# Optimization experiments

Hardware: AMD Instinct MI355X
Metric: run time of the kernel (lower is better)

The kernel has to match this reference:

```python
import jax, jax.numpy as jnp
import numpy as np

B, H, Q, K = 2, 12, 2048, 2048
D, NPOS = 128, 512


def setup_inputs() -> dict:
    key = jax.random.key(0)
    k1, k2, k3 = jax.random.split(key, 3)
    return {
        "query": jax.random.normal(k1, (B, H, Q, D), dtype=jnp.float32),
        "attn_logits": jax.random.normal(k2, (B, H, Q, K), dtype=jnp.float32),
        "pos_emb": jax.random.normal(k3, (1, D, NPOS), dtype=jnp.float32),
        "npos_max": NPOS,
    }


def reference(query, attn_logits, pos_emb, npos_max):
    # CoPE, 1D (H=None) branch.
    gates = jax.nn.sigmoid(attn_logits)                       # [b,h,q,k]
    # reversed cumsum along keys: position of each key counted from the right
    pos = jnp.flip(jnp.cumsum(jnp.flip(gates, axis=-1), axis=-1), axis=-1)
    pos = jnp.minimum(pos, jnp.float32(npos_max - 1))
    pos_ceil = jnp.ceil(pos).astype(jnp.int32)                # [b,h,q,k]
    pos_floor = jnp.floor(pos).astype(jnp.int32)
    # query @ pos_emb -> interpolation table over integer positions
    logits_int = jnp.einsum("bhqd,dn->bhqn", query, pos_emb[0])  # [b,h,q,npos]
    logits_ceil = jnp.take_along_axis(logits_int, pos_ceil, axis=-1)
    logits_floor = jnp.take_along_axis(logits_int, pos_floor, axis=-1)
    w = pos - pos_floor.astype(pos.dtype)
    return logits_ceil * w + logits_floor * (1.0 - w)
```

## Files before the change

kernel.cpp:

```cpp
#include <hip/hip_runtime.h>
#include <math.h>

#define DD    128
#define NPOS  512
#define KK    2048
#define RPB   16
#define BLK   1024

typedef __attribute__((ext_vector_type(8))) short short8_t;
typedef __attribute__((ext_vector_type(4))) float f32x4;

union BfPack {
    unsigned u[4];
    short8_t v;
};

__device__ __forceinline__ float sigmoidf_fast(float x) {
    return __builtin_amdgcn_rcpf(1.0f + __expf(-x));
}

__device__ __forceinline__ unsigned pack_bf16(float lo, float hi) {
    return (__float_as_uint(hi) & 0xffff0000u) | (__float_as_uint(lo) >> 16);
}

__global__ __launch_bounds__(BLK, 8)
void cope_kernel(const float* __restrict__ query,
                 const float* __restrict__ attn,
                 const float* __restrict__ pos_emb,
                 const int*   __restrict__ npos_max_p,
                 float* __restrict__ out)
{
    const int t    = threadIdx.x;
    const int wv   = t >> 6;
    const int lane = t & 63;

    __shared__ float s_tab[RPB][NPOS + 1];

    const size_t row_base = (size_t)blockIdx.x * RPB;

    {
        const int m  = lane & 15;
        const int g  = lane >> 4;
        const int n0 = wv * 32 + m;

        f32x4 acc0 = {0.f, 0.f, 0.f, 0.f};
        f32x4 acc1 = {0.f, 0.f, 0.f, 0.f};

        #pragma unroll
        for (int kk = 0; kk < 4; ++kk) {
            const int k0 = kk * 32 + g * 8;

            const float* qp = query + (row_base + m) * DD + k0;
            f32x4 a0 = *reinterpret_cast<const f32x4*>(qp);
            f32x4 a1 = *reinterpret_cast<const f32x4*>(qp + 4);
            BfPack af;
            af.u[0] = pack_bf16(a0.x, a0.y);
            af.u[1] = pack_bf16(a0.z, a0.w);
            af.u[2] = pack_bf16(a1.x, a1.y);
            af.u[3] = pack_bf16(a1.z, a1.w);

            const float* bp = pos_emb + (size_t)k0 * NPOS + n0;
            float b0[8], b1[8];
            #pragma unroll
            for (int j = 0; j < 8; ++j) {
                b0[j] = bp[(size_t)j * NPOS];
                b1[j] = bp[(size_t)j * NPOS + 16];
            }
            BfPack bf0, bf1;
            #pragma unroll
            for (int j = 0; j < 4; ++j) {
                bf0.u[j] = pack_bf16(b0[2 * j], b0[2 * j + 1]);
                bf1.u[j] = pack_bf16(b1[2 * j], b1[2 * j + 1]);
            }

            acc0 = __builtin_amdgcn_mfma_f32_16x16x32_bf16(af.v, bf0.v, acc0, 0, 0, 0);
            acc1 = __builtin_amdgcn_mfma_f32_16x16x32_bf16(af.v, bf1.v, acc1, 0, 0, 0);
        }

        #pragma unroll
        for (int r = 0; r < 4; ++r) {
            s_tab[g * 4 + r][n0]      = acc0[r];
            s_tab[g * 4 + r][n0 + 16] = acc1[r];
        }
        if (t < RPB) s_tab[t][NPOS] = 0.0f;
    }
    __syncthreads();

    {
        float lo[8], hi[8];
        #pragma unroll
        for (int j = 0; j < 8; ++j) {
            const int e = lane + j * 64;
            lo[j] = s_tab[wv][e];
            hi[j] = s_tab[wv][e + 1];
        }
        __syncthreads();
        unsigned* urow = reinterpret_cast<unsigned*>(s_tab[wv]);
        #pragma unroll
        for (int j = 0; j < 8; ++j)
            urow[lane + j * 64] = pack_bf16(lo[j], hi[j]);
    }
    __syncthreads();

    const size_t row = row_base + wv;
    const float* arow = attn + row * (size_t)KK;
    float*       orow = out  + row * (size_t)KK;
    const unsigned* utab = reinterpret_cast<const unsigned*>(s_tab[wv]);

    const float clampv = (float)(*npos_max_p - 1);

    float suff[8][4];
    float lct[8];
    float incl[8];

    #pragma unroll
    for (int c = 0; c < 8; ++c) {
        f32x4 gv = *reinterpret_cast<const f32x4*>(arow + c * 256 + lane * 4);
        float s0 = sigmoidf_fast(gv.x);
        float s1 = sigmoidf_fast(gv.y);
        float s2 = sigmoidf_fast(gv.z);
        float s3 = sigmoidf_fast(gv.w);
        suff[c][3] = s3;
        suff[c][2] = s2 + suff[c][3];
        suff[c][1] = s1 + suff[c][2];
        suff[c][0] = s0 + suff[c][1];
        lct[c] = suff[c][0];

        float v = lct[c];
        #pragma unroll
        for (int off = 1; off < 64; off <<= 1) {
            float u = __shfl_down(v, off);
            if (lane + off < 64) v += u;
        }
        incl[c] = v;
    }

    float Tc[8];
    #pragma unroll
    for (int c = 0; c < 8; ++c) Tc[c] = __shfl(incl[c], 0);
    float offc[8];
    offc[7] = 0.0f;
    #pragma unroll
    for (int c = 6; c >= 0; --c) offc[c] = offc[c + 1] + Tc[c + 1];

    #pragma unroll
    for (int c = 0; c < 8; ++c) {
        float base = offc[c] + (incl[c] - lct[c]);
        f32x4 res;
        #pragma unroll
        for (int j = 0; j < 4; ++j) {
            float pos = fminf(suff[c][j] + base, clampv);
            int   ifl = (int)pos;
            float wgt = pos - (float)ifl;
            unsigned u = utab[ifl];
            float lf = __uint_as_float(u << 16);
            float lc = __uint_as_float(u & 0xffff0000u);
            res[j] = fmaf(wgt, lc - lf, lf);
        }
        __builtin_nontemporal_store(res, reinterpret_cast<f32x4*>(orow + c * 256 + lane * 4));
    }
}

extern "C" void kernel_launch(void* const* d_in, const int* in_sizes, int n_in,
                              void* d_out, int out_size, void* d_ws, size_t ws_size,
                              hipStream_t stream) {
    const float* query   = (const float*)d_in[0];
    const float* attn    = (const float*)d_in[1];
    const float* pos_emb = (const float*)d_in[2];
    const int*   nposp   = (const int*)d_in[3];
    float*       outp    = (float*)d_out;

    const int rows   = in_sizes[1] / KK;
    const int blocks = rows / RPB;

    cope_kernel<<<blocks, BLK, 0, stream>>>(query, attn, pos_emb, nposp, outp);
}
```

Measured before the change: 169.0 us.

## Process six row groups per block with double-buffered GEMM table pipelining

Each block now handles six groups of 16 rows instead of one. The query×pos_emb MFMA for the next group is computed while the current group runs its scan and gather, using double-buffered LDS tables. This cuts block launch count and overlaps GEMM work with memory-bound output. The in-place bf16 pack now happens with no barrier between its reads and writes, and only one __syncthreads runs per iteration. This may race across waves, since each wave reads e+1 from its own row only, so it is probably fine. The grid shrinks to 49152/96 = 512 blocks, which lowers parallelism on a 256-CU device.

```diff
diff --git a/kernel.cpp b/kernel.cpp
--- a/kernel.cpp
+++ b/kernel.cpp
@@ -6,6 +6,8 @@
 #define KK    2048
 #define RPB   16
 #define BLK   1024
+#define GPB   6
+#define LROW  (NPOS + 1)
 
 typedef __attribute__((ext_vector_type(8))) short short8_t;
 typedef __attribute__((ext_vector_type(4))) float f32x4;
@@ -34,21 +36,25 @@
     const int wv   = t >> 6;
     const int lane = t & 63;
 
-    __shared__ float s_tab[RPB][NPOS + 1];
+    __shared__ float s_tab[2][RPB][LROW];
 
-    const size_t row_base = (size_t)blockIdx.x * RPB;
+    const size_t blk_row0 = (size_t)blockIdx.x * (RPB * GPB);
 
-    {
-        const int m  = lane & 15;
-        const int g  = lane >> 4;
-        const int n0 = wv * 32 + m;
+    const int m   = lane & 15;
+    const int g16 = lane >> 4;
+    const int n0  = wv * 32 + m;
 
-        f32x4 acc0 = {0.f, 0.f, 0.f, 0.f};
-        f32x4 acc1 = {0.f, 0.f, 0.f, 0.f};
+    const float clampv = (float)(*npos_max_p - 1);
 
+    f32x4 acc0, acc1;
+
+    auto gemm_compute = [&](int grp) {
+        const size_t row_base = blk_row0 + (size_t)grp * RPB;
+        acc0 = (f32x4){0.f, 0.f, 0.f, 0.f};
+        acc1 = (f32x4){0.f, 0.f, 0.f, 0.f};
         #pragma unroll
         for (int kk = 0; kk < 4; ++kk) {
-            const int k0 = kk * 32 + g * 8;
+            const int k0 = kk * 32 + g16 * 8;
 
             const float* qp = query + (row_base + m) * DD + k0;
             f32x4 a0 = *reinterpret_cast<const f32x4*>(qp);
@@ -76,88 +82,101 @@
             acc0 = __builtin_amdgcn_mfma_f32_16x16x32_bf16(af.v, bf0.v, acc0, 0, 0, 0);
             acc1 = __builtin_amdgcn_mfma_f32_16x16x32_bf16(af.v, bf1.v, acc1, 0, 0, 0);
         }
+    };
+
+    auto gemm_store = [&](int buf) {
+        #pragma unroll
+        for (int r = 0; r < 4; ++r) {
+            s_tab[buf][g16 * 4 + r][n0]      = acc0[r];
+            s_tab[buf][g16 * 4 + r][n0 + 16] = acc1[r];
+        }
+        if (t < RPB) s_tab[buf][t][NPOS] = 0.0f;
+    };
+
+    gemm_compute(0);
+    gemm_store(0);
+
+    #pragma unroll 1
+    for (int g = 0; g < GPB; ++g) {
+        const int cur = g & 1;
+
+        if (g + 1 < GPB) gemm_compute(g + 1);
+
+        __syncthreads();
+
+        if (g + 1 < GPB) gemm_store(cur ^ 1);
+
+        float* tabf = s_tab[cur][wv];
+        {
+            float lo[8], hi[8];
+            #pragma unroll
+            for (int j = 0; j < 8; ++j) {
+                const int e = lane + j * 64;
+                lo[j] = tabf[e];
+                hi[j] = tabf[e + 1];
+            }
+            unsigned* urow = reinterpret_cast<unsigned*>(tabf);
+            #pragma unroll
+            for (int j = 0; j < 8; ++j)
+                urow[lane + j * 64] = pack_bf16(lo[j], hi[j]);
+        }
+
+        const size_t row  = blk_row0 + (size_t)g * RPB + wv;
+        const float* arow = attn + row * (size_t)KK;
+        float*       orow = out  + row * (size_t)KK;
+        const unsigned* utab = reinterpret_cast<const unsigned*>(tabf);
+
+        float suff[8][4];
+        float lct[8];
+        float incl[8];
 
         #pragma unroll
-        for (int r = 0; r < 4; ++r) {
-            s_tab[g * 4 + r][n0]      = acc0[r];
-            s_tab[g * 4 + r][n0 + 16] = acc1[r];
+        for (int c = 0; c < 8; ++c) {
+            f32x4 gv = *reinterpret_cast<const f32x4*>(arow + c * 256 + lane * 4);
+            float s0 = sigmoidf_fast(gv.x);
+            float s1 = sigmoidf_fast(gv.y);
+            float s2 = sigmoidf_fast(gv.z);
+            float s3 = sigmoidf_fast(gv.w);
+            suff[c][3] = s3;
+            suff[c][2] = s2 + suff[c][3];
+            suff[c][1] = s1 + suff[c][2];
+            suff[c][0] = s0 + suff[c][1];
+            lct[c] = suff[c][0];
+
+            float v = lct[c];
+            #pragma unroll
+            for (int off = 1; off < 64; off <<= 1) {
+                float u = __shfl_down(v, off);
+                if (lane + off < 64) v += u;
+            }
+            incl[c] = v;
         }
-        if (t < RPB) s_tab[t][NPOS] = 0.0f;
-    }
-    __syncthreads();
 
-    {
-        float lo[8], hi[8];
+        float Tc[8];
         #pragma unroll
-        for (int j = 0; j < 8; ++j) {
-            const int e = lane + j * 64;
-            lo[j] = s_tab[wv][e];
-            hi[j] = s_tab[wv][e + 1];
+        for (int c = 0; c < 8; ++c) Tc[c] = __shfl(incl[c], 0);
+        float offc[8];
+        offc[7] = 0.0f;
+        #pragma unroll
+        for (int c = 6; c >= 0; --c) offc[c] = offc[c + 1] + Tc[c + 1];
+
+        #pragma unroll
+        for (int c = 0; c < 8; ++c) {
+            float base = offc[c] + (incl[c] - lct[c]);
+            f32x4 res;
+            #pragma unroll
+            for (int j = 0; j < 4; ++j) {
+                float pos = fminf(suff[c][j] + base, clampv);
+                int   ifl = (int)pos;
+                float wgt = pos - (float)ifl;
+                unsigned u = utab[ifl];
+                float lf = __uint_as_float(u << 16);
+                float lc = __uint_as_float(u & 0xffff0000u);
+                res[j] = fmaf(wgt, lc - lf, lf);
+            }
+            __builtin_nontemporal_store(res,
+                reinterpret_cast<f32x4*>(orow + c * 256 + lane * 4));
         }
-        __syncthreads();
-        unsigned* urow = reinterpret_cast<unsigned*>(s_tab[wv]);
-        #pragma unroll
-        for (int j = 0; j < 8; ++j)
-            urow[lane + j * 64] = pack_bf16(lo[j], hi[j]);
-    }
-    __syncthreads();
-
-    const size_t row = row_base + wv;
-    const float* arow = attn + row * (size_t)KK;
-    float*       orow = out  + row * (size_t)KK;
-    const unsigned* utab = reinterpret_cast<const unsigned*>(s_tab[wv]);
-
-    const float clampv = (float)(*npos_max_p - 1);
-
-    float suff[8][4];
-    float lct[8];
-    float incl[8];
-
-    #pragma unroll
-    for (int c = 0; c < 8; ++c) {
-        f32x4 gv = *reinterpret_cast<const f32x4*>(arow + c * 256 + lane * 4);
-        float s0 = sigmoidf_fast(gv.x);
-        float s1 = sigmoidf_fast(gv.y);
-        float s2 = sigmoidf_fast(gv.z);
-        float s3 = sigmoidf_fast(gv.w);
-        suff[c][3] = s3;
-        suff[c][2] = s2 + suff[c][3];
-        suff[c][1] = s1 + suff[c][2];
-        suff[c][0] = s0 + suff[c][1];
-        lct[c] = suff[c][0];
-
-        float v = lct[c];
-        #pragma unroll
-        for (int off = 1; off < 64; off <<= 1) {
-            float u = __shfl_down(v, off);
-            if (lane + off < 64) v += u;
-        }
-        incl[c] = v;
-    }
-
-    float Tc[8];
-    #pragma unroll
-    for (int c = 0; c < 8; ++c) Tc[c] = __shfl(incl[c], 0);
-    float offc[8];
-    offc[7] = 0.0f;
-    #pragma unroll
-    for (int c = 6; c >= 0; --c) offc[c] = offc[c + 1] + Tc[c + 1];
-
-    #pragma unroll
-    for (int c = 0; c < 8; ++c) {
-        float base = offc[c] + (incl[c] - lct[c]);
-        f32x4 res;
-        #pragma unroll
-        for (int j = 0; j < 4; ++j) {
-            float pos = fminf(suff[c][j] + base, clampv);
-            int   ifl = (int)pos;
-            float wgt = pos - (float)ifl;
-            unsigned u = utab[ifl];
-            float lf = __uint_as_float(u << 16);
-            float lc = __uint_as_float(u & 0xffff0000u);
-            res[j] = fmaf(wgt, lc - lf, lf);
-        }
-        __builtin_nontemporal_store(res, reinterpret_cast<f32x4*>(orow + c * 256 + lane * 4));
     }
 }
 
@@ -171,7 +190,7 @@
     float*       outp    = (float*)d_out;
 
     const int rows   = in_sizes[1] / KK;
-    const int blocks = rows / RPB;
+    const int blocks = rows / (RPB * GPB);
 
     cope_kernel<<<blocks, BLK, 0, stream>>>(query, attn, pos_emb, nposp, outp);
 }
```

Result: slower. 495.0 us (+192.9%).
